# Performance work log

Hardware: AMD Instinct MI355X
Metric: run time of the kernel (lower is better)

Reference implementation:

```python
import jax, jax.numpy as jnp
import numpy as np

B, T, E, H = 2, 2048, 1024, 16
HD = E // H
EPS = 1e-5


def layer_norm(x, g, b):
    mu = jnp.mean(x, axis=-1, keepdims=True)
    var = jnp.mean(jnp.square(x - mu), axis=-1, keepdims=True)
    return (x - mu) * jax.lax.rsqrt(var + EPS) * g + b


def setup_inputs() -> dict:
    key = jax.random.key(0)
    ks = jax.random.split(key, 12)
    s = 0.02
    return {
        "x": jax.random.normal(ks[0], (B, T, E), jnp.float32),
        "Wk": jax.random.normal(ks[1], (E, E), jnp.float32) * s,
        "Wq": jax.random.normal(ks[2], (E, E), jnp.float32) * s,
        "Wv": jax.random.normal(ks[3], (E, E), jnp.float32) * s,
        "Wp": jax.random.normal(ks[4], (E, E), jnp.float32) * s,
        "bp": jnp.zeros((E,), jnp.float32),
        "W1": jax.random.normal(ks[5], (E, 4 * E), jnp.float32) * s,
        "b1": jnp.zeros((4 * E,), jnp.float32),
        "W2": jax.random.normal(ks[6], (4 * E, E), jnp.float32) * s,
        "b2": jnp.zeros((E,), jnp.float32),
        "g1": jnp.ones((E,), jnp.float32),
        "be1": jnp.zeros((E,), jnp.float32),
        "g2": jnp.ones((E,), jnp.float32),
        "be2": jnp.zeros((E,), jnp.float32),
    }


def reference(x, Wk, Wq, Wv, Wp, bp, W1, b1, W2, b2, g1, be1, g2, be2):
    # --- attention sublayer ---
    h = layer_norm(x, g1, be1)
    q = (h @ Wq).reshape(B, T, H, HD).transpose(0, 2, 1, 3)  # [B,H,T,HD]
    k = (h @ Wk).reshape(B, T, H, HD).transpose(0, 2, 1, 3)
    v = (h @ Wv).reshape(B, T, H, HD).transpose(0, 2, 1, 3)
    scores = jnp.einsum('bhqd,bhkd->bhqk', q, k) * (HD ** -0.5)
    causal = jnp.tril(jnp.ones((T, T), bool))
    scores = jnp.where(causal, scores, -jnp.inf)
    probs = jax.nn.softmax(scores, axis=-1)  # dropout is identity (eval)
    attn = jnp.einsum('bhqk,bhkd->bhqd', probs, v)
    attn = attn.transpose(0, 2, 1, 3).reshape(B, T, E)
    x = x + attn @ Wp + bp
    # --- FFN sublayer ---
    h2 = layer_norm(x, g2, be2)
    ff = jax.nn.relu(h2 @ W1 + b1) @ W2 + b2
    return x + ff
```

## Files before the change

### kernel.cpp

```cpp
#include <hip/hip_runtime.h>
#include <hip/hip_bf16.h>

#define B_ 2
#define T_ 2048
#define E_ 1024
#define H_ 16
#define HD_ 64
#define NT (B_*T_)

typedef __attribute__((ext_vector_type(8))) short s16x8;
typedef __attribute__((ext_vector_type(4))) float f32x4;
typedef __attribute__((ext_vector_type(4))) unsigned int u32x4;

using bf16 = __hip_bfloat16;

#define MFMA16(a,b,c) __builtin_amdgcn_mfma_f32_16x16x32_bf16(a,b,c,0,0,0)

__device__ inline unsigned short f2bf(float f) {
    bf16 h = __float2bfloat16(f);
    return *reinterpret_cast<unsigned short*>(&h);
}

__device__ __forceinline__ unsigned cvt_pk_bf16(float lo, float hi) {
    unsigned r;
    asm("v_cvt_pk_bf16_f32 %0, %1, %2" : "=v"(r) : "v"(lo), "v"(hi));
    return r;
}

__device__ __forceinline__ void async_cp16(const void* g, void* l) {
    __builtin_amdgcn_global_load_lds((const __attribute__((address_space(1))) void*)g,
                                     (__attribute__((address_space(3))) void*)l,
                                     16, 0, 0);
}

__global__ __launch_bounds__(256) void transpose_all(const float* __restrict__ Wq,
                                                     const float* __restrict__ Wk,
                                                     const float* __restrict__ Wv,
                                                     const float* __restrict__ Wp,
                                                     const float* __restrict__ W1,
                                                     const float* __restrict__ W2,
                                                     bf16* __restrict__ Wqkv_t,
                                                     bf16* __restrict__ W1_t,
                                                     bf16* __restrict__ W2_t) {
    __shared__ float tile[32][33];
    int id = blockIdx.x;
    const float* src; bf16* dst; int K, N, n0, k0;
    if (id < 4096) {
        int z = id >> 10, t = id & 1023;
        src = z == 0 ? Wq : z == 1 ? Wk : z == 2 ? Wv : Wp;
        dst = Wqkv_t + (size_t)z * 1048576;
        K = 1024; N = 1024; n0 = (t & 31) * 32; k0 = (t >> 5) * 32;
    } else if (id < 8192) {
        int t = id - 4096; src = W1; dst = W1_t; K = 1024; N = 4096;
        n0 = (t & 127) * 32; k0 = (t >> 7) * 32;
    } else {
        int t = id - 8192; src = W2; dst = W2_t; K = 4096; N = 1024;
        n0 = (t & 31) * 32; k0 = (t >> 5) * 32;
    }
    int tx = threadIdx.x, ty = threadIdx.y;
#pragma unroll
    for (int i = 0; i < 4; ++i)
        tile[ty + i*8][tx] = src[(size_t)(k0 + ty + i*8)*N + n0 + tx];
    __syncthreads();
#pragma unroll
    for (int i = 0; i < 4; ++i)
        dst[(size_t)(n0 + ty + i*8)*K + k0 + tx] = __float2bfloat16(tile[tx][ty + i*8]);
}

__global__ __launch_bounds__(256) void ln_kernel(const float* __restrict__ x,
                                                 const float* __restrict__ g,
                                                 const float* __restrict__ b,
                                                 bf16* __restrict__ h) {
    int row = blockIdx.x;
    int tid = threadIdx.x;
    const float4 xv = *reinterpret_cast<const float4*>(x + (size_t)row*E_ + tid*4);
    float s  = xv.x + xv.y + xv.z + xv.w;
    float sq = xv.x*xv.x + xv.y*xv.y + xv.z*xv.z + xv.w*xv.w;
#pragma unroll
    for (int o = 32; o > 0; o >>= 1) { s += __shfl_xor(s, o); sq += __shfl_xor(sq, o); }
    __shared__ float red[8];
    int w = tid >> 6, lane = tid & 63;
    if (lane == 0) { red[w] = s; red[4 + w] = sq; }
    __syncthreads();
    float S = red[0] + red[1] + red[2] + red[3];
    float Q = red[4] + red[5] + red[6] + red[7];
    float mu = S * (1.0f/E_);
    float var = Q * (1.0f/E_) - mu*mu;
    float rs = rsqrtf(var + 1e-5f);
    const float4 gv = *reinterpret_cast<const float4*>(g + tid*4);
    const float4 bv = *reinterpret_cast<const float4*>(b + tid*4);
    ushort4 o4;
    o4.x = f2bf((xv.x - mu)*rs*gv.x + bv.x);
    o4.y = f2bf((xv.y - mu)*rs*gv.y + bv.y);
    o4.z = f2bf((xv.z - mu)*rs*gv.z + bv.z);
    o4.w = f2bf((xv.w - mu)*rs*gv.w + bv.w);
    *reinterpret_cast<ushort4*>(h + (size_t)row*E_ + tid*4) = o4;
}

template<int BN, int EPI>
__global__ __launch_bounds__(256)
void gemm_t(const bf16* __restrict__ A, const bf16* __restrict__ Bt, void* Cout,
            const float* __restrict__ bias, const float* res,
            int M, int N, int K) {
    constexpr int NB = BN / 32;
    constexpr int HALF = BN / 2;
    __shared__ bf16 As[128*64];
    __shared__ bf16 Bs[BN*64];
    int tid = threadIdx.x;
    int lane = tid & 63, w = tid >> 6;
    int wr = w >> 1, wc = w & 1;
    int nbx = gridDim.x;
    int hid = blockIdx.y * nbx + blockIdx.x;
    int cpx = (nbx * gridDim.y) >> 3;
    int nid = (hid & 7) * cpx + (hid >> 3);
    int m0 = (nid / nbx) * 128, n0 = (nid % nbx) * BN;
    int lr = lane & 15, lq = lane >> 4;
    f32x4 acc[4][NB] = {};
    int srow = w*8 + (lane >> 3);
    int schunk = ((lane & 7) ^ (srow & 7)) * 8;
    const bf16* Ap = A  + (size_t)(m0 + srow)*K + schunk;
    const bf16* Bp = Bt + (size_t)(n0 + srow)*K + schunk;
    for (int k0 = 0; k0 < K; k0 += 64) {
#pragma unroll
        for (int i = 0; i < 4; ++i)
            async_cp16(Ap + (size_t)(i*32)*K + k0, (char*)As + i*4096 + w*1024);
#pragma unroll
        for (int i = 0; i < BN/32; ++i)
            async_cp16(Bp + (size_t)(i*32)*K + k0, (char*)Bs + i*4096 + w*1024);
        __syncthreads();
        const char* Asb = (const char*)As;
        const char* Bsb = (const char*)Bs;
        s16x8 af[2][4], bfr[2][NB];
#pragma unroll
        for (int m = 0; m < 4; ++m) {
            int row = wr*64 + m*16 + lr;
            int base = row*128, sw = (row & 7) << 4;
#pragma unroll
            for (int kk = 0; kk < 2; ++kk)
                af[kk][m] = *reinterpret_cast<const s16x8*>(Asb + base + ((kk*64 + lq*16) ^ sw));
        }
#pragma unroll
        for (int n = 0; n < NB; ++n) {
            int row = wc*HALF + n*16 + lr;
            int base = row*128, sw = (row & 7) << 4;
#pragma unroll
            for (int kk = 0; kk < 2; ++kk)
                bfr[kk][n] = *reinterpret_cast<const s16x8*>(Bsb + base + ((kk*64 + lq*16) ^ sw));
        }
        __builtin_amdgcn_s_setprio(1);
#pragma unroll
        for (int kk = 0; kk < 2; ++kk)
#pragma unroll
            for (int m = 0; m < 4; ++m)
#pragma unroll
                for (int n = 0; n < NB; ++n)
                    acc[m][n] = MFMA16(af[kk][m], bfr[kk][n], acc[m][n]);
        __builtin_amdgcn_s_setprio(0);
        __syncthreads();
    }
#pragma unroll
    for (int m = 0; m < 4; ++m) {
#pragma unroll
        for (int n = 0; n < NB; ++n) {
            int col = n0 + wc*HALF + n*16 + lr;
#pragma unroll
            for (int r = 0; r < 4; ++r) {
                int row = m0 + wr*64 + m*16 + lq*4 + r;
                float v = acc[m][n][r];
                if (EPI == 0) {
                    reinterpret_cast<bf16*>(Cout)[(size_t)row*N + col] = __float2bfloat16(v);
                } else if (EPI == 1) {
                    reinterpret_cast<float*>(Cout)[(size_t)row*N + col] =
                        v + bias[col] + res[(size_t)row*N + col];
                } else {
                    v += bias[col];
                    v = v > 0.f ? v : 0.f;
                    reinterpret_cast<bf16*>(Cout)[(size_t)row*N + col] = __float2bfloat16(v);
                }
            }
        }
    }
}

__global__ __launch_bounds__(256) void v_transpose(const bf16* __restrict__ qkv,
                                                   bf16* __restrict__ Vt) {
    __shared__ unsigned short tile[32][33];
    int tx = threadIdx.x, ty = threadIdx.y;
    int bh = blockIdx.z;
    int b = bh >> 4, h = bh & 15;
    int t0 = blockIdx.x * 32, d0 = blockIdx.y * 32;
    const unsigned short* src = reinterpret_cast<const unsigned short*>(qkv);
#pragma unroll
    for (int i = 0; i < 4; ++i)
        tile[ty + i*8][tx] = src[(size_t)(b*T_ + t0 + ty + i*8)*3072 + 2048 + h*64 + d0 + tx];
    __syncthreads();
    unsigned short* dst = reinterpret_cast<unsigned short*>(Vt);
#pragma unroll
    for (int i = 0; i < 4; ++i)
        dst[(size_t)(bh*64 + d0 + ty + i*8)*T_ + t0 + tx] = tile[tx][ty + i*8];
}

__global__ __launch_bounds__(256)
void flash_attn(const bf16* __restrict__ qkv, const bf16* __restrict__ Vt,
                bf16* __restrict__ O) {
    __shared__ char smem[40960];
    int tid = threadIdx.x;
    int lane = tid & 63, w = tid >> 6;
    int lr = lane & 15, lq = lane >> 4;
    int bh = blockIdx.y, b = bh >> 4, h = bh & 15;
    int qt = (int)((blockIdx.x + blockIdx.y) & 31);
    int q0 = qt * 64;
    int qw = q0 + w * 16;
    const bf16* Qb = qkv + (size_t)(b*T_)*3072 + h*HD_;
    const bf16* Kb = Qb + 1024;
    const bf16* Vb = Vt + (size_t)bh * HD_ * T_;
    char* Pw = smem + 32768 + w*2048;

    int sc_   = (((lane & 7) ^ ((lane >> 3) & 7))) * 8;
    int srow_ = w*8 + (lane >> 3);

    s16x8 qf[2];
#pragma unroll
    for (int kk = 0; kk < 2; ++kk)
        qf[kk] = *reinterpret_cast<const s16x8*>(Qb + (size_t)(qw + lr)*3072 + kk*32 + lq*8);
    f32x4 od[4] = {};
    float lrun = 0.f;
    const float SLOG2E = 0.125f * 1.44269504088896f;
    int ntiles = qt + 1;

#define STAGE(bufi, tile) do {                                                          \
        int kv0s_ = (tile) * 64;                                                        \
        _Pragma("unroll")                                                               \
        for (int i_ = 0; i_ < 2; ++i_) {                                                \
            int rr_ = i_*32 + srow_;                                                    \
            async_cp16(Kb + (size_t)(kv0s_ + rr_)*3072 + sc_,                           \
                       smem + (bufi)*8192 + i_*4096 + w*1024);                          \
            async_cp16(Vb + (size_t)rr_*2048 + kv0s_ + sc_,                             \
                       smem + 16384 + (bufi)*8192 + i_*4096 + w*1024);                  \
        } } while (0)

    STAGE(0, 0);
    for (int it = 0; it < ntiles; ++it) {
        int curb = it & 1;
        int kv0 = it * 64;
        if (it + 1 < ntiles) {
            STAGE(curb ^ 1, it + 1);
            asm volatile("s_waitcnt vmcnt(4)" ::: "memory");
        } else {
            asm volatile("s_waitcnt vmcnt(0)" ::: "memory");
        }
        __builtin_amdgcn_sched_barrier(0);
        __builtin_amdgcn_s_barrier();
        __builtin_amdgcn_sched_barrier(0);
        const char* Kt = smem + curb*8192;
        const char* Vtl = smem + 16384 + curb*8192;
        f32x4 sc[4];
        __builtin_amdgcn_s_setprio(1);
#pragma unroll
        for (int n = 0; n < 4; ++n) {
            int row = n*16 + lr;
            int ko = row*128 + ((lq ^ (row & 7)) << 4);
            s16x8 kf0 = *reinterpret_cast<const s16x8*>(Kt + ko);
            s16x8 kf1 = *reinterpret_cast<const s16x8*>(Kt + (ko ^ 64));
            f32x4 z = {0.f, 0.f, 0.f, 0.f};
            z = MFMA16(kf0, qf[0], z);
            z = MFMA16(kf1, qf[1], z);
            sc[n] = z;
        }
        __builtin_amdgcn_s_setprio(0);
        if (it == ntiles - 1) {
            int q = qw + lr;
#pragma unroll
            for (int n = 0; n < 4; ++n)
#pragma unroll
                for (int r = 0; r < 4; ++r)
                    if (kv0 + n*16 + lq*4 + r > q) sc[n][r] = -1e30f;
        }
        float psum = 0.f;
#pragma unroll
        for (int n = 0; n < 4; ++n) {
            float p0 = exp2f(sc[n][0] * SLOG2E);
            float p1 = exp2f(sc[n][1] * SLOG2E);
            float p2 = exp2f(sc[n][2] * SLOG2E);
            float p3 = exp2f(sc[n][3] * SLOG2E);
            psum += (p0 + p1) + (p2 + p3);
            uint2 pk;
            pk.x = cvt_pk_bf16(p0, p1);
            pk.y = cvt_pk_bf16(p2, p3);
            int bo = (lr*128 + n*32 + lq*8) ^ ((lr & 7) << 4);
            *reinterpret_cast<uint2*>(Pw + bo) = pk;
        }
        psum += __shfl_xor(psum, 16);
        psum += __shfl_xor(psum, 32);
        lrun += psum;
        asm volatile("" ::: "memory");
        s16x8 pa[2];
#pragma unroll
        for (int kk = 0; kk < 2; ++kk) {
            int bo = (lr*128 + kk*64 + lq*16) ^ ((lr & 7) << 4);
            pa[kk] = *reinterpret_cast<const s16x8*>(Pw + bo);
        }
        __builtin_amdgcn_s_setprio(1);
#pragma unroll
        for (int nd = 0; nd < 4; ++nd) {
            int row = nd*16 + lr;
            int vo = row*128 + ((lq ^ (row & 7)) << 4);
            s16x8 vf0 = *reinterpret_cast<const s16x8*>(Vtl + vo);
            s16x8 vf1 = *reinterpret_cast<const s16x8*>(Vtl + (vo ^ 64));
            od[nd] = MFMA16(pa[0], vf0, od[nd]);
            od[nd] = MFMA16(pa[1], vf1, od[nd]);
        }
        __builtin_amdgcn_s_setprio(0);
        __builtin_amdgcn_sched_barrier(0);
        __builtin_amdgcn_s_barrier();
        __builtin_amdgcn_sched_barrier(0);
    }
#undef STAGE
    float lR[4];
#pragma unroll
    for (int r = 0; r < 4; ++r) lR[r] = 1.0f / __shfl(lrun, lq*4 + r);
#pragma unroll
    for (int nd = 0; nd < 4; ++nd) {
#pragma unroll
        for (int r = 0; r < 4; ++r) {
            int row = qw + lq*4 + r;
            O[(size_t)(b*T_ + row)*E_ + h*HD_ + nd*16 + lr] = __float2bfloat16(od[nd][r] * lR[r]);
        }
    }
}

extern "C" void kernel_launch(void* const* d_in, const int* in_sizes, int n_in,
                              void* d_out, int out_size, void* d_ws, size_t ws_size,
                              hipStream_t stream) {
    const float* x   = (const float*)d_in[0];
    const float* Wk  = (const float*)d_in[1];
    const float* Wq  = (const float*)d_in[2];
    const float* Wv  = (const float*)d_in[3];
    const float* Wp  = (const float*)d_in[4];
    const float* bp  = (const float*)d_in[5];
    const float* W1  = (const float*)d_in[6];
    const float* b1  = (const float*)d_in[7];
    const float* W2  = (const float*)d_in[8];
    const float* b2  = (const float*)d_in[9];
    const float* g1  = (const float*)d_in[10];
    const float* be1 = (const float*)d_in[11];
    const float* g2  = (const float*)d_in[12];
    const float* be2 = (const float*)d_in[13];
    float* out = (float*)d_out;

    char* ws = (char*)d_ws;
    bf16* Wqkv_t = (bf16*)(ws + 0);
    bf16* Wp_t   = (bf16*)(ws + 6291456);
    bf16* W1_t   = (bf16*)(ws + 8388608);
    bf16* W2_t   = (bf16*)(ws + 16777216);
    bf16* h      = (bf16*)(ws + 25165824);
    bf16* qkv    = (bf16*)(ws + 33554432);
    bf16* Vt     = (bf16*)(ws + 58720256);
    bf16* attnO  = (bf16*)(ws + 67108864);
    bf16* ff1    = (bf16*)(ws + 33554432);
    float* x2    = (ws_size >= 92274688) ? (float*)(ws + 75497472) : out;

    dim3 tb(32, 8);
    transpose_all<<<12288, tb, 0, stream>>>(Wq, Wk, Wv, Wp, W1, W2, Wqkv_t, W1_t, W2_t);

    ln_kernel<<<NT, 256, 0, stream>>>(x, g1, be1, h);
    gemm_t<128,0><<<dim3(24, 32), 256, 0, stream>>>(h, Wqkv_t, qkv, nullptr, nullptr, NT, 3072, 1024);
    v_transpose<<<dim3(64, 2, 32), tb, 0, stream>>>(qkv, Vt);
    flash_attn<<<dim3(32, 32), 256, 0, stream>>>(qkv, Vt, attnO);
    gemm_t<64,1><<<dim3(16, 32), 256, 0, stream>>>(attnO, Wp_t, x2, bp, x, NT, 1024, 1024);
    ln_kernel<<<NT, 256, 0, stream>>>(x2, g2, be2, h);
    gemm_t<128,2><<<dim3(32, 32), 256, 0, stream>>>(h, W1_t, ff1, b1, nullptr, NT, 4096, 1024);
    gemm_t<64,1><<<dim3(16, 32), 256, 0, stream>>>(ff1, W2_t, out, b2, x2, NT, 1024, 4096);
}
```

Measured before the change: 227.0 us.

## Double-buffer shared memory in BN=64 GEMMs to overlap loads with MFMA

Adds a template flag that enables two shared-memory buffers in the GEMM kernel. The next K-tile is loaded asynchronously while the current one is computed, with explicit vmcnt waits and raw barriers in place of __syncthreads. It is enabled only for the two BN=64 GEMMs (output projection and FFN down-projection), where the synchronous load-then-compute loop leaves the matrix units idle during global loads. The cost is twice the LDS per block, which may lower occupancy, plus hand-counted vmcnt values that depend on the number of copies issued per stage.

Result: slower. 243.6 us (+7.3%).

```diff
diff --git a/kernel.cpp b/kernel.cpp
--- a/kernel.cpp
+++ b/kernel.cpp
@@ -97,15 +97,17 @@
     *reinterpret_cast<ushort4*>(h + (size_t)row*E_ + tid*4) = o4;
 }
 
-template<int BN, int EPI>
+template<int BN, int EPI, bool PF>
 __global__ __launch_bounds__(256)
 void gemm_t(const bf16* __restrict__ A, const bf16* __restrict__ Bt, void* Cout,
             const float* __restrict__ bias, const float* res,
             int M, int N, int K) {
     constexpr int NB = BN / 32;
     constexpr int HALF = BN / 2;
-    __shared__ bf16 As[128*64];
-    __shared__ bf16 Bs[BN*64];
+    constexpr int NBUF = PF ? 2 : 1;
+    constexpr int AISS = 4, BISS = BN/32;
+    __shared__ bf16 As[NBUF*128*64];
+    __shared__ bf16 Bs[NBUF*BN*64];
     int tid = threadIdx.x;
     int lane = tid & 63, w = tid >> 6;
     int wr = w >> 1, wc = w & 1;
@@ -120,16 +122,18 @@
     int schunk = ((lane & 7) ^ (srow & 7)) * 8;
     const bf16* Ap = A  + (size_t)(m0 + srow)*K + schunk;
     const bf16* Bp = Bt + (size_t)(n0 + srow)*K + schunk;
-    for (int k0 = 0; k0 < K; k0 += 64) {
-#pragma unroll
-        for (int i = 0; i < 4; ++i)
-            async_cp16(Ap + (size_t)(i*32)*K + k0, (char*)As + i*4096 + w*1024);
-#pragma unroll
-        for (int i = 0; i < BN/32; ++i)
-            async_cp16(Bp + (size_t)(i*32)*K + k0, (char*)Bs + i*4096 + w*1024);
-        __syncthreads();
-        const char* Asb = (const char*)As;
-        const char* Bsb = (const char*)Bs;
+
+    auto stage = [&](int buf, int k0) {
+#pragma unroll
+        for (int i = 0; i < AISS; ++i)
+            async_cp16(Ap + (size_t)(i*32)*K + k0, (char*)As + buf*16384 + i*4096 + w*1024);
+#pragma unroll
+        for (int i = 0; i < BISS; ++i)
+            async_cp16(Bp + (size_t)(i*32)*K + k0, (char*)Bs + buf*(BN*128) + i*4096 + w*1024);
+    };
+    auto compute = [&](int buf) {
+        const char* Asb = (const char*)As + buf*16384;
+        const char* Bsb = (const char*)Bs + buf*(BN*128);
         s16x8 af[2][4], bfr[2][NB];
 #pragma unroll
         for (int m = 0; m < 4; ++m) {
@@ -156,7 +160,35 @@
                 for (int n = 0; n < NB; ++n)
                     acc[m][n] = MFMA16(af[kk][m], bfr[kk][n], acc[m][n]);
         __builtin_amdgcn_s_setprio(0);
-        __syncthreads();
+    };
+
+    if (PF) {
+        int nsteps = K >> 6;
+        stage(0, 0);
+        for (int s = 0; s < nsteps; ++s) {
+            int cur = s & 1;
+            if (s + 1 < nsteps) {
+                stage(cur ^ 1, (s + 1) << 6);
+                if (BN == 64) asm volatile("s_waitcnt vmcnt(6)" ::: "memory");
+                else          asm volatile("s_waitcnt vmcnt(8)" ::: "memory");
+            } else {
+                asm volatile("s_waitcnt vmcnt(0)" ::: "memory");
+            }
+            __builtin_amdgcn_sched_barrier(0);
+            __builtin_amdgcn_s_barrier();
+            __builtin_amdgcn_sched_barrier(0);
+            compute(cur);
+            __builtin_amdgcn_sched_barrier(0);
+            __builtin_amdgcn_s_barrier();
+            __builtin_amdgcn_sched_barrier(0);
+        }
+    } else {
+        for (int k0 = 0; k0 < K; k0 += 64) {
+            stage(0, k0);
+            __syncthreads();
+            compute(0);
+            __syncthreads();
+        }
     }
 #pragma unroll
     for (int m = 0; m < 4; ++m) {
@@ -364,11 +396,11 @@
     transpose_all<<<12288, tb, 0, stream>>>(Wq, Wk, Wv, Wp, W1, W2, Wqkv_t, W1_t, W2_t);
 
     ln_kernel<<<NT, 256, 0, stream>>>(x, g1, be1, h);
-    gemm_t<128,0><<<dim3(24, 32), 256, 0, stream>>>(h, Wqkv_t, qkv, nullptr, nullptr, NT, 3072, 1024);
+    gemm_t<128,0,false><<<dim3(24, 32), 256, 0, stream>>>(h, Wqkv_t, qkv, nullptr, nullptr, NT, 3072, 1024);
     v_transpose<<<dim3(64, 2, 32), tb, 0, stream>>>(qkv, Vt);
     flash_attn<<<dim3(32, 32), 256, 0, stream>>>(qkv, Vt, attnO);
-    gemm_t<64,1><<<dim3(16, 32), 256, 0, stream>>>(attnO, Wp_t, x2, bp, x, NT, 1024, 1024);
+    gemm_t<64,1,true><<<dim3(16, 32), 256, 0, stream>>>(attnO, Wp_t, x2, bp, x, NT, 1024, 1024);
     ln_kernel<<<NT, 256, 0, stream>>>(x2, g2, be2, h);
-    gemm_t<128,2><<<dim3(32, 32), 256, 0, stream>>>(h, W1_t, ff1, b1, nullptr, NT, 4096, 1024);
-    gemm_t<64,1><<<dim3(16, 32), 256, 0, stream>>>(ff1, W2_t, out, b2, x2, NT, 1024, 4096);
-}
+    gemm_t<128,2,false><<<dim3(32, 32), 256, 0, stream>>>(h, W1_t, ff1, b1, nullptr, NT, 4096, 1024);
+    gemm_t<64,1,true><<<dim3(16, 32), 256, 0, stream>>>(ff1, W2_t, out, b2, x2, NT, 1024, 4096);
+}
```
